# Performance work log

Measured on AMD Instinct MI355X. Metric: run time of the kernel, lower is better.

Reference implementation:

```python
import jax, jax.numpy as jnp
import numpy as np

D_MODEL = 768
BATCH = 2
N_CTX = 4096


def setup_inputs() -> dict:
    key = jax.random.key(0)
    k1, k2 = jax.random.split(key)
    x = jax.random.normal(k1, (BATCH, N_CTX, D_MODEL), dtype=jnp.float32)
    # proj: Linear(d_model, 3*d_model, bias=False); torch stores weight as [out, in]
    W_proj = jax.random.normal(k2, (3 * D_MODEL, D_MODEL), dtype=jnp.float32) * (1.0 / np.sqrt(D_MODEL))
    return {"x": x, "W_proj": W_proj}


def reference(x, W_proj):
    d = x.shape[-1]
    n_ctx = x.shape[-2]
    # qkv: [B, S, 3D] = x @ W^T (torch Linear semantics)
    qkv = jnp.einsum("bsd,ed->bse", x, W_proj)
    Q, K, V = jnp.split(qkv, 3, axis=-1)
    # additive causal mask: 0 on/below diagonal, -inf above (1 - 1/tril(ones))
    causal = jnp.tril(jnp.ones((n_ctx, n_ctx), dtype=bool))
    mask = jnp.where(causal, 0.0, -jnp.inf).astype(x.dtype)
    # NOTE: no 1/sqrt(d) scaling in the original module
    scores = jnp.einsum("bqd,bkd->bqk", Q, K) + mask
    attn = jax.nn.softmax(scores, axis=-1)
    out = x + jnp.einsum("bqk,bkd->bqd", attn, V)
    return out
```

## Files before the change

### kernel.cpp

```cpp
#include <hip/hip_runtime.h>
#include <hip/hip_bf16.h>
#include <hip/hip_fp16.h>

typedef _Float16 f16;
typedef _Float16 f16x8 __attribute__((ext_vector_type(8)));
typedef _Float16 f16x4 __attribute__((ext_vector_type(4)));
typedef _Float16 f16x2 __attribute__((ext_vector_type(2)));
typedef float f32x4 __attribute__((ext_vector_type(4)));

#define D_MODEL 768
#define S_CTX   4096
#define NBATCH  2
#define M_TOK   (NBATCH * S_CTX)
#define N3      (3 * D_MODEL)

__device__ __forceinline__ void gload_lds16(const void* g, void* l) {
  __builtin_amdgcn_global_load_lds(
      (__attribute__((address_space(1))) unsigned int*)g,
      (__attribute__((address_space(3))) unsigned int*)l, 16, 0, 0);
}

__global__ __launch_bounds__(256) void cvt_f32_f16(const float* __restrict__ s,
                                                   f16* __restrict__ d, int n4) {
  int i = blockIdx.x * 256 + threadIdx.x;
  if (i >= n4) return;
  f32x4 v = ((const f32x4*)s)[i];
  f16x4 h;
  h[0] = (f16)v[0]; h[1] = (f16)v[1]; h[2] = (f16)v[2]; h[3] = (f16)v[3];
  ((f16x4*)d)[i] = h;
}

__global__ __launch_bounds__(256, 2) void proj_gemm(
    const f16* __restrict__ A, const f16* __restrict__ B,
    f16* __restrict__ qh, f16* __restrict__ kh, f16* __restrict__ vth) {
  __shared__ f16 As[128 * 32];
  __shared__ f16 Bs[128 * 32];

  const int tid  = threadIdx.x;
  const int w    = tid >> 6, lane = tid & 63;
  const int wr   = w >> 1,   wc   = w & 1;
  const int bm0  = blockIdx.x * 128, bn0 = blockIdx.y * 128;
  const int srow = lane >> 2;
  const int scol = (lane & 3) * 8;

  f32x4 acc[4][4] = {};

  const f16* gA = A + (size_t)bm0 * 768;
  const f16* gB = B + (size_t)bn0 * 768;

  for (int kt = 0; kt < 24; ++kt) {
    __syncthreads();
    const int k0 = kt * 32 + scol;
#pragma unroll
    for (int cc = 0; cc < 2; ++cc) {
      int c = w + cc * 4;
      gload_lds16(gA + (size_t)(c * 16 + srow) * 768 + k0, (char*)As + c * 1024);
      gload_lds16(gB + (size_t)(c * 16 + srow) * 768 + k0, (char*)Bs + c * 1024);
    }
    __syncthreads();

    const int fr = lane & 15, fk = (lane >> 4) * 8;
    f16x8 af[4], bf[4];
#pragma unroll
    for (int i = 0; i < 4; ++i)
      af[i] = *(const f16x8*)(As + (wr * 64 + i * 16 + fr) * 32 + fk);
#pragma unroll
    for (int j = 0; j < 4; ++j)
      bf[j] = *(const f16x8*)(Bs + (wc * 64 + j * 16 + fr) * 32 + fk);
#pragma unroll
    for (int i = 0; i < 4; ++i)
#pragma unroll
      for (int j = 0; j < 4; ++j)
        acc[i][j] = __builtin_amdgcn_mfma_f32_16x16x32_f16(af[i], bf[j], acc[i][j], 0, 0, 0);
  }

  const int fr = lane & 15, fq = lane >> 4;
#pragma unroll
  for (int i = 0; i < 4; ++i) {
#pragma unroll
    for (int j = 0; j < 4; ++j) {
      int gn      = bn0 + wc * 64 + j * 16 + fr;
      int gm_base = bm0 + wr * 64 + i * 16 + fq * 4;
      if (gn < 1536) {
        f16* dst = (gn < 768) ? qh : kh;
        int  col = (gn < 768) ? gn : gn - 768;
#pragma unroll
        for (int r = 0; r < 4; ++r)
          dst[(size_t)(gm_base + r) * 768 + col] = (f16)acc[i][j][r];
      } else {
        int d = gn - 1536;
        int bb = gm_base >> 12, s = gm_base & 4095;
        f16x4 h;
        h[0] = (f16)acc[i][j][0]; h[1] = (f16)acc[i][j][1];
        h[2] = (f16)acc[i][j][2]; h[3] = (f16)acc[i][j][3];
        *(f16x4*)(vth + ((size_t)bb * 768 + d) * 4096 + s) = h;
      }
    }
  }
}

#define SM_K0   0
#define SM_K1   49152
#define SM_V    98304
#define SM_SS   147456
#define SM_PS   155648
#define SM_M    157696
#define SM_L    157824
#define SM_F    157952
#define SM_SZ   158080

__global__ __launch_bounds__(512, 2) void attn_part(
    const f16* __restrict__ qg, const f16* __restrict__ kg,
    const f16* __restrict__ vt, f16* __restrict__ p0,
    float* __restrict__ p1, float* __restrict__ ml) {
  extern __shared__ __align__(16) char smem[];
  char*  Kb0 = smem + SM_K0;
  char*  Kb1 = smem + SM_K1;
  char*  Vb  = smem + SM_V;
  float* Ss0 = (float*)(smem + SM_SS);
  float* Ss1 = Ss0 + 1024;
  char*  Ps  = smem + SM_PS;
  float* mS  = (float*)(smem + SM_M);
  float* lS  = (float*)(smem + SM_L);
  float* fS  = (float*)(smem + SM_F);

  const int tid  = threadIdx.x;
  const int wv   = tid >> 6, lane = tid & 63;
  const int fr   = lane & 15, fq = lane >> 4;
  const int qi   = wv >> 2, ki = (wv >> 1) & 1, dh = wv & 1;

  const int u = blockIdx.x;
  int vv = (u < 256) ? u : (u - 256);
  const int qb = ((u < 256) ? 127 : 63) - (vv >> 2);
  const int b  = (vv >> 1) & 1;
  const int c  = vv & 1;
  const int q0 = qb * 32;
  const int n  = (q0 >> 5) + 1;
  const int n0 = (n + 1) >> 1;
  const int ts = c ? n0 : 0;
  const int te = c ? n : n0;

  const char* kbase = (const char*)(kg + (size_t)b * 4096 * 768);
  const char* vbase = (const char*)(vt + (size_t)b * 768 * 4096);

  f16x8 qreg[12];
  {
    const f16* qp = qg + ((size_t)b * 4096 + q0 + qi * 16 + fr) * 768 + dh * 384 + fq * 8;
#pragma unroll
    for (int kk = 0; kk < 12; ++kk) qreg[kk] = *(const f16x8*)(qp + kk * 32);
  }

  if (tid < 32) { mS[tid] = -1e30f; lS[tid] = 0.f; }

  f32x4 acc[2][6] = {};

  if (ts < te) {
    const char* kb = kbase + (size_t)(ts * 32) * 1536;
    char* dst = (ts & 1) ? Kb1 : Kb0;
#pragma unroll
    for (int i = 0; i < 6; ++i) {
      int lin = wv * 6144 + i * 1024 + lane * 16;
      int row = lin / 1536, cb = lin - row * 1536;
      gload_lds16(kb + (size_t)row * 1536 + (cb ^ ((row & 7) << 4)),
                  dst + wv * 6144 + i * 1024);
    }
  }
  asm volatile("s_waitcnt vmcnt(0)" ::: "memory");
  __builtin_amdgcn_s_barrier();

  for (int t = ts; t < te; ++t) {
    const int kv0 = t * 32;
    const bool pf = (t + 1 < te);

    {
      const char* vb = vbase + (size_t)kv0 * 2;
#pragma unroll
      for (int i = 0; i < 6; ++i) {
        int lin = wv * 6144 + i * 1024 + lane * 16;
        int d = lin >> 6, cb = lin & 63;
        gload_lds16(vb + (size_t)d * 8192 + (cb ^ (((d >> 1) & 3) << 4)),
                    Vb + wv * 6144 + i * 1024);
      }
    }
    if (pf) {
      const char* kb = kbase + (size_t)(kv0 + 32) * 1536;
      char* dst = ((t + 1) & 1) ? Kb1 : Kb0;
#pragma unroll
      for (int i = 0; i < 6; ++i) {
        int lin = wv * 6144 + i * 1024 + lane * 16;
        int row = lin / 1536, cb = lin - row * 1536;
        gload_lds16(kb + (size_t)row * 1536 + (cb ^ ((row & 7) << 4)),
                    dst + wv * 6144 + i * 1024);
      }
    }

    {
      const char* kbuf = (t & 1) ? Kb1 : Kb0;
      f32x4 sc = {};
      const int krow = ki * 16 + fr;
      const int kswz = (krow & 7) << 4;
      __builtin_amdgcn_s_setprio(1);
#pragma unroll
      for (int kk = 0; kk < 12; ++kk) {
        int by = krow * 1536 + dh * 768 + kk * 64 + fq * 16;
        f16x8 kf = *(const f16x8*)(kbuf + (by ^ kswz));
        sc = __builtin_amdgcn_mfma_f32_16x16x32_f16(qreg[kk], kf, sc, 0, 0, 0);
      }
      __builtin_amdgcn_s_setprio(0);
      float* sdst = (dh ? Ss1 : Ss0) + (qi * 16 + fq * 4) * 32 + ki * 16 + fr;
#pragma unroll
      for (int r = 0; r < 4; ++r) sdst[r * 32] = sc[r];
    }
    asm volatile("s_waitcnt lgkmcnt(0)" ::: "memory");
    __builtin_amdgcn_s_barrier();

    {
      const int row = tid >> 4, sub = tid & 15;
      const int c0 = sub * 2;
      float a0 = Ss0[row * 32 + c0]     + Ss1[row * 32 + c0];
      float a1 = Ss0[row * 32 + c0 + 1] + Ss1[row * 32 + c0 + 1];
      const int grow = q0 + row;
      if (kv0 + c0     > grow) a0 = -1e30f;
      if (kv0 + c0 + 1 > grow) a1 = -1e30f;
      float mx = fmaxf(a0, a1);
      mx = fmaxf(mx, __shfl_xor(mx, 1));
      mx = fmaxf(mx, __shfl_xor(mx, 2));
      mx = fmaxf(mx, __shfl_xor(mx, 4));
      mx = fmaxf(mx, __shfl_xor(mx, 8));
      float mo = mS[row];
      float mn = fmaxf(mo, mx);
      float p0v = __expf(a0 - mn), p1v = __expf(a1 - mn);
      float sum = p0v + p1v;
      sum += __shfl_xor(sum, 1);
      sum += __shfl_xor(sum, 2);
      sum += __shfl_xor(sum, 4);
      sum += __shfl_xor(sum, 8);
      if (sub == 0) {
        float f = __expf(mo - mn);
        mS[row] = mn; fS[row] = f; lS[row] = lS[row] * f + sum;
      }
      f16x2 ph; ph[0] = (f16)p0v; ph[1] = (f16)p1v;
      int by = row * 64 + sub * 4;
      *(f16x2*)(Ps + (by ^ (((row >> 1) & 3) << 4))) = ph;
    }
    asm volatile("s_waitcnt lgkmcnt(0)" ::: "memory");
    __builtin_amdgcn_s_barrier();

    {
      f32x4 f0 = *(const f32x4*)(fS + fq * 4);
      f32x4 f1 = *(const f32x4*)(fS + 16 + fq * 4);
#pragma unroll
      for (int ct = 0; ct < 6; ++ct)
#pragma unroll
        for (int r = 0; r < 4; ++r) {
          acc[0][ct][r] *= f0[r];
          acc[1][ct][r] *= f1[r];
        }
      int byA0 = (fr * 64 + fq * 16) ^ (((fr >> 1) & 3) << 4);
      int rb = 16 + fr;
      int byA1 = (rb * 64 + fq * 16) ^ (((rb >> 1) & 3) << 4);
      f16x8 pa0 = *(const f16x8*)(Ps + byA0);
      f16x8 pa1 = *(const f16x8*)(Ps + byA1);
      if (pf) { asm volatile("s_waitcnt vmcnt(6)" ::: "memory"); }
      else    { asm volatile("s_waitcnt vmcnt(0)" ::: "memory"); }
      __builtin_amdgcn_s_setprio(1);
#pragma unroll
      for (int ct = 0; ct < 6; ++ct) {
        int d = wv * 96 + ct * 16 + fr;
        int by = (d * 64 + fq * 16) ^ (((d >> 1) & 3) << 4);
        f16x8 bv = *(const f16x8*)(Vb + by);
        acc[0][ct] = __builtin_amdgcn_mfma_f32_16x16x32_f16(pa0, bv, acc[0][ct], 0, 0, 0);
        acc[1][ct] = __builtin_amdgcn_mfma_f32_16x16x32_f16(pa1, bv, acc[1][ct], 0, 0, 0);
      }
      __builtin_amdgcn_s_setprio(0);
    }
    asm volatile("s_waitcnt vmcnt(0) lgkmcnt(0)" ::: "memory");
    __builtin_amdgcn_s_barrier();
  }

  const size_t obase = (size_t)b * 4096 + q0;
  if (c == 0) {
#pragma unroll
    for (int ct = 0; ct < 6; ++ct) {
      int d = wv * 96 + ct * 16 + fr;
#pragma unroll
      for (int r = 0; r < 4; ++r) {
        p0[(obase + fq * 4 + r) * 768 + d]      = (f16)acc[0][ct][r];
        p0[(obase + 16 + fq * 4 + r) * 768 + d] = (f16)acc[1][ct][r];
      }
    }
  } else {
#pragma unroll
    for (int ct = 0; ct < 6; ++ct) {
      int d = wv * 96 + ct * 16 + fr;
#pragma unroll
      for (int r = 0; r < 4; ++r) {
        p1[(obase + fq * 4 + r) * 768 + d]      = acc[0][ct][r];
        p1[(obase + 16 + fq * 4 + r) * 768 + d] = acc[1][ct][r];
      }
    }
  }
  if (tid < 32) {
    float* mlp = ml + ((size_t)(c * 2 + b) * 4096 + q0 + tid) * 2;
    mlp[0] = mS[tid];
    mlp[1] = lS[tid];
  }
}

__global__ __launch_bounds__(256) void attn_combine(
    const float* __restrict__ x, const f16* __restrict__ p0,
    const float* __restrict__ ml, float* __restrict__ out) {
  int i = blockIdx.x * 256 + threadIdx.x;
  int row = i / 192;
  int b = row >> 12, s = row & 4095;
  const float* m0p = ml + ((size_t)b * 4096 + s) * 2;
  const float* m1p = ml + ((size_t)(2 + b) * 4096 + s) * 2;
  float m0 = m0p[0], l0 = m0p[1];
  float m1 = m1p[0], l1 = m1p[1];
  float m  = fmaxf(m0, m1);
  float f0 = __expf(m0 - m), f1 = __expf(m1 - m);
  float inv = 1.f / (l0 * f0 + l1 * f1);
  f32x4 a1 = ((const f32x4*)out)[i];
  f16x4 a0 = ((const f16x4*)p0)[i];
  f32x4 xv = ((const f32x4*)x)[i];
  f32x4 o;
#pragma unroll
  for (int r = 0; r < 4; ++r)
    o[r] = xv[r] + ((float)a0[r] * f0 + a1[r] * f1) * inv;
  ((f32x4*)out)[i] = o;
}

extern "C" void kernel_launch(void* const* d_in, const int* in_sizes, int n_in,
                              void* d_out, int out_size, void* d_ws, size_t ws_size,
                              hipStream_t stream) {
  const float* x  = (const float*)d_in[0];
  const float* Wp = (const float*)d_in[1];
  float* out = (float*)d_out;

  char* ws = (char*)d_ws;
  f16* x_h  = (f16*)(ws);
  f16* w_h  = (f16*)(ws + 12582912);
  f16* q_h  = (f16*)(ws + 16121856);
  f16* k_h  = (f16*)(ws + 28704768);
  f16* vt_h = (f16*)(ws + 41287680);

  f16*   p0 = x_h;
  float* ml = (float*)w_h;

  hipFuncSetAttribute(reinterpret_cast<const void*>(attn_part),
                      hipFuncAttributeMaxDynamicSharedMemorySize, SM_SZ);

  cvt_f32_f16<<<(M_TOK * D_MODEL) / 1024, 256, 0, stream>>>(x, x_h, (M_TOK * D_MODEL) / 4);
  cvt_f32_f16<<<(N3 * D_MODEL) / 1024, 256, 0, stream>>>(Wp, w_h, (N3 * D_MODEL) / 4);
  proj_gemm<<<dim3(64, 18), 256, 0, stream>>>(x_h, w_h, q_h, k_h, vt_h);
  attn_part<<<512, 512, SM_SZ, stream>>>(q_h, k_h, vt_h, p0, out, ml);
  attn_combine<<<(M_TOK * D_MODEL) / 1024, 256, 0, stream>>>(x, p0, ml, out);
}
```

Before: 240.2 us.

## Software-pipeline attention loop: QK^T one tile ahead, V straight to registers

Restructures the flash-attention partial kernel so that QK^T for tile t+1 and the K prefetch for tile t+2 are issued while softmax for tile t runs. This cuts the per-iteration barriers from three to two and double-buffers the score buffer. V is no longer staged through LDS; it is loaded directly from global memory into double-buffered registers, shrinking the LDS footprint. It also splits the QK^T accumulation into two independent MFMA chains and skips the accumulator rescale when no row max changed, at the cost of more register pressure and more delicate vmcnt bookkeeping.

```diff
diff --git a/kernel.cpp b/kernel.cpp
--- a/kernel.cpp
+++ b/kernel.cpp
@@ -101,28 +101,22 @@
 
 #define SM_K0   0
 #define SM_K1   49152
-#define SM_V    98304
-#define SM_SS   147456
-#define SM_PS   155648
-#define SM_M    157696
-#define SM_L    157824
-#define SM_F    157952
-#define SM_SZ   158080
+#define SM_SS   98304
+#define SM_PS   114688
+#define SM_M    116736
+#define SM_L    116864
+#define SM_F    116992
+#define SM_SZ   117120
 
 __global__ __launch_bounds__(512, 2) void attn_part(
     const f16* __restrict__ qg, const f16* __restrict__ kg,
     const f16* __restrict__ vt, f16* __restrict__ p0,
     float* __restrict__ p1, float* __restrict__ ml) {
   extern __shared__ __align__(16) char smem[];
-  char*  Kb0 = smem + SM_K0;
-  char*  Kb1 = smem + SM_K1;
-  char*  Vb  = smem + SM_V;
-  float* Ss0 = (float*)(smem + SM_SS);
-  float* Ss1 = Ss0 + 1024;
-  char*  Ps  = smem + SM_PS;
-  float* mS  = (float*)(smem + SM_M);
-  float* lS  = (float*)(smem + SM_L);
-  float* fS  = (float*)(smem + SM_F);
+  char*  Ps = smem + SM_PS;
+  float* mS = (float*)(smem + SM_M);
+  float* lS = (float*)(smem + SM_L);
+  float* fS = (float*)(smem + SM_F);
 
   const int tid  = threadIdx.x;
   const int wv   = tid >> 6, lane = tid & 63;
@@ -141,7 +135,7 @@
   const int te = c ? n : n0;
 
   const char* kbase = (const char*)(kg + (size_t)b * 4096 * 768);
-  const char* vbase = (const char*)(vt + (size_t)b * 768 * 4096);
+  const f16*  vbase = vt + (size_t)b * 768 * 4096;
 
   f16x8 qreg[12];
   {
@@ -153,10 +147,11 @@
   if (tid < 32) { mS[tid] = -1e30f; lS[tid] = 0.f; }
 
   f32x4 acc[2][6] = {};
-
-  if (ts < te) {
-    const char* kb = kbase + (size_t)(ts * 32) * 1536;
-    char* dst = (ts & 1) ? Kb1 : Kb0;
+  f16x8 vA[6], vB[6];
+
+  auto stageK = [&](int t) {
+    const char* kb = kbase + (size_t)(t * 32) * 1536;
+    char* dst = smem + ((t & 1) ? SM_K1 : SM_K0);
 #pragma unroll
     for (int i = 0; i < 6; ++i) {
       int lin = wv * 6144 + i * 1024 + lane * 16;
@@ -164,118 +159,128 @@
       gload_lds16(kb + (size_t)row * 1536 + (cb ^ ((row & 7) << 4)),
                   dst + wv * 6144 + i * 1024);
     }
-  }
-  asm volatile("s_waitcnt vmcnt(0)" ::: "memory");
-  __builtin_amdgcn_s_barrier();
-
-  for (int t = ts; t < te; ++t) {
+  };
+
+  auto loadV = [&](int t, f16x8 (&vr)[6]) {
+    const f16* vp = vbase + (size_t)(wv * 96 + fr) * 4096 + t * 32 + fq * 8;
+#pragma unroll
+    for (int ct = 0; ct < 6; ++ct)
+      vr[ct] = *(const f16x8*)(vp + (size_t)ct * 16 * 4096);
+  };
+
+  auto qkt = [&](int t) {
+    const char* kb = smem + ((t & 1) ? SM_K1 : SM_K0);
+    const int krow = ki * 16 + fr;
+    const int kswz = (krow & 7) << 4;
+    f32x4 sa = {}, sb = {};
+#pragma unroll
+    for (int kk = 0; kk < 12; kk += 2) {
+      int by = krow * 1536 + dh * 768 + kk * 64 + fq * 16;
+      f16x8 k0 = *(const f16x8*)(kb + (by ^ kswz));
+      f16x8 k1 = *(const f16x8*)(kb + ((by + 64) ^ kswz));
+      sa = __builtin_amdgcn_mfma_f32_16x16x32_f16(qreg[kk],     k0, sa, 0, 0, 0);
+      sb = __builtin_amdgcn_mfma_f32_16x16x32_f16(qreg[kk + 1], k1, sb, 0, 0, 0);
+    }
+    sa = sa + sb;
+    float* sdst = (float*)(smem + SM_SS + ((t & 1) ? 8192 : 0) + dh * 4096)
+                  + (qi * 16 + fq * 4) * 32 + ki * 16 + fr;
+#pragma unroll
+    for (int r = 0; r < 4; ++r) sdst[r * 32] = sa[r];
+  };
+
+  auto softmax_f = [&](int t) {
     const int kv0 = t * 32;
-    const bool pf = (t + 1 < te);
-
-    {
-      const char* vb = vbase + (size_t)kv0 * 2;
-#pragma unroll
-      for (int i = 0; i < 6; ++i) {
-        int lin = wv * 6144 + i * 1024 + lane * 16;
-        int d = lin >> 6, cb = lin & 63;
-        gload_lds16(vb + (size_t)d * 8192 + (cb ^ (((d >> 1) & 3) << 4)),
-                    Vb + wv * 6144 + i * 1024);
-      }
-    }
-    if (pf) {
-      const char* kb = kbase + (size_t)(kv0 + 32) * 1536;
-      char* dst = ((t + 1) & 1) ? Kb1 : Kb0;
-#pragma unroll
-      for (int i = 0; i < 6; ++i) {
-        int lin = wv * 6144 + i * 1024 + lane * 16;
-        int row = lin / 1536, cb = lin - row * 1536;
-        gload_lds16(kb + (size_t)row * 1536 + (cb ^ ((row & 7) << 4)),
-                    dst + wv * 6144 + i * 1024);
-      }
-    }
-
-    {
-      const char* kbuf = (t & 1) ? Kb1 : Kb0;
-      f32x4 sc = {};
-      const int krow = ki * 16 + fr;
-      const int kswz = (krow & 7) << 4;
-      __builtin_amdgcn_s_setprio(1);
-#pragma unroll
-      for (int kk = 0; kk < 12; ++kk) {
-        int by = krow * 1536 + dh * 768 + kk * 64 + fq * 16;
-        f16x8 kf = *(const f16x8*)(kbuf + (by ^ kswz));
-        sc = __builtin_amdgcn_mfma_f32_16x16x32_f16(qreg[kk], kf, sc, 0, 0, 0);
-      }
-      __builtin_amdgcn_s_setprio(0);
-      float* sdst = (dh ? Ss1 : Ss0) + (qi * 16 + fq * 4) * 32 + ki * 16 + fr;
-#pragma unroll
-      for (int r = 0; r < 4; ++r) sdst[r * 32] = sc[r];
-    }
+    const float* S0 = (const float*)(smem + SM_SS + ((t & 1) ? 8192 : 0));
+    const float* S1 = S0 + 1024;
+    const int row = tid >> 4, sub = tid & 15;
+    const int c0 = sub * 2;
+    float a0 = S0[row * 32 + c0]     + S1[row * 32 + c0];
+    float a1 = S0[row * 32 + c0 + 1] + S1[row * 32 + c0 + 1];
+    const int grow = q0 + row;
+    if (kv0 + c0     > grow) a0 = -1e30f;
+    if (kv0 + c0 + 1 > grow) a1 = -1e30f;
+    float mx = fmaxf(a0, a1);
+    mx = fmaxf(mx, __shfl_xor(mx, 1));
+    mx = fmaxf(mx, __shfl_xor(mx, 2));
+    mx = fmaxf(mx, __shfl_xor(mx, 4));
+    mx = fmaxf(mx, __shfl_xor(mx, 8));
+    float mo = mS[row];
+    float mn = fmaxf(mo, mx);
+    float p0v = __expf(a0 - mn), p1v = __expf(a1 - mn);
+    float sum = p0v + p1v;
+    sum += __shfl_xor(sum, 1);
+    sum += __shfl_xor(sum, 2);
+    sum += __shfl_xor(sum, 4);
+    sum += __shfl_xor(sum, 8);
+    if (sub == 0) {
+      float f = __expf(mo - mn);
+      mS[row] = mn; fS[row] = f; lS[row] = lS[row] * f + sum;
+    }
+    f16x2 ph; ph[0] = (f16)p0v; ph[1] = (f16)p1v;
+    int by = row * 64 + sub * 4;
+    *(f16x2*)(Ps + (by ^ (((row >> 1) & 3) << 4))) = ph;
+  };
+
+  auto ITER = [&](int t, f16x8 (&vCon)[6], f16x8 (&vNxt)[6]) {
+    const bool haveN1 = (t + 1 < te);
+    const bool haveN2 = (t + 2 < te);
+    asm volatile("s_waitcnt vmcnt(6)" ::: "memory");
+    __builtin_amdgcn_s_barrier();
+    if (haveN2) stageK(t + 2);
+    asm volatile("" ::: "memory");
+    if (haveN1) loadV(t + 1, vNxt);
+    asm volatile("" ::: "memory");
+    if (haveN1) qkt(t + 1);
+    softmax_f(t);
     asm volatile("s_waitcnt lgkmcnt(0)" ::: "memory");
     __builtin_amdgcn_s_barrier();
-
-    {
-      const int row = tid >> 4, sub = tid & 15;
-      const int c0 = sub * 2;
-      float a0 = Ss0[row * 32 + c0]     + Ss1[row * 32 + c0];
-      float a1 = Ss0[row * 32 + c0 + 1] + Ss1[row * 32 + c0 + 1];
-      const int grow = q0 + row;
-      if (kv0 + c0     > grow) a0 = -1e30f;
-      if (kv0 + c0 + 1 > grow) a1 = -1e30f;
-      float mx = fmaxf(a0, a1);
-      mx = fmaxf(mx, __shfl_xor(mx, 1));
-      mx = fmaxf(mx, __shfl_xor(mx, 2));
-      mx = fmaxf(mx, __shfl_xor(mx, 4));
-      mx = fmaxf(mx, __shfl_xor(mx, 8));
-      float mo = mS[row];
-      float mn = fmaxf(mo, mx);
-      float p0v = __expf(a0 - mn), p1v = __expf(a1 - mn);
-      float sum = p0v + p1v;
-      sum += __shfl_xor(sum, 1);
-      sum += __shfl_xor(sum, 2);
-      sum += __shfl_xor(sum, 4);
-      sum += __shfl_xor(sum, 8);
-      if (sub == 0) {
-        float f = __expf(mo - mn);
-        mS[row] = mn; fS[row] = f; lS[row] = lS[row] * f + sum;
-      }
-      f16x2 ph; ph[0] = (f16)p0v; ph[1] = (f16)p1v;
-      int by = row * 64 + sub * 4;
-      *(f16x2*)(Ps + (by ^ (((row >> 1) & 3) << 4))) = ph;
-    }
-    asm volatile("s_waitcnt lgkmcnt(0)" ::: "memory");
-    __builtin_amdgcn_s_barrier();
-
     {
       f32x4 f0 = *(const f32x4*)(fS + fq * 4);
       f32x4 f1 = *(const f32x4*)(fS + 16 + fq * 4);
-#pragma unroll
-      for (int ct = 0; ct < 6; ++ct)
-#pragma unroll
-        for (int r = 0; r < 4; ++r) {
-          acc[0][ct][r] *= f0[r];
-          acc[1][ct][r] *= f1[r];
-        }
+      bool nd = (f0[0] < 1.f) || (f0[1] < 1.f) || (f0[2] < 1.f) || (f0[3] < 1.f) ||
+                (f1[0] < 1.f) || (f1[1] < 1.f) || (f1[2] < 1.f) || (f1[3] < 1.f);
+      if (__any(nd)) {
+#pragma unroll
+        for (int ct = 0; ct < 6; ++ct)
+#pragma unroll
+          for (int r = 0; r < 4; ++r) {
+            acc[0][ct][r] *= f0[r];
+            acc[1][ct][r] *= f1[r];
+          }
+      }
       int byA0 = (fr * 64 + fq * 16) ^ (((fr >> 1) & 3) << 4);
       int rb = 16 + fr;
       int byA1 = (rb * 64 + fq * 16) ^ (((rb >> 1) & 3) << 4);
       f16x8 pa0 = *(const f16x8*)(Ps + byA0);
       f16x8 pa1 = *(const f16x8*)(Ps + byA1);
-      if (pf) { asm volatile("s_waitcnt vmcnt(6)" ::: "memory"); }
-      else    { asm volatile("s_waitcnt vmcnt(0)" ::: "memory"); }
+      if (haveN2)      { asm volatile("s_waitcnt vmcnt(12)" ::: "memory"); }
+      else if (haveN1) { asm volatile("s_waitcnt vmcnt(6)"  ::: "memory"); }
+      else             { asm volatile("s_waitcnt vmcnt(0)"  ::: "memory"); }
       __builtin_amdgcn_s_setprio(1);
 #pragma unroll
       for (int ct = 0; ct < 6; ++ct) {
-        int d = wv * 96 + ct * 16 + fr;
-        int by = (d * 64 + fq * 16) ^ (((d >> 1) & 3) << 4);
-        f16x8 bv = *(const f16x8*)(Vb + by);
-        acc[0][ct] = __builtin_amdgcn_mfma_f32_16x16x32_f16(pa0, bv, acc[0][ct], 0, 0, 0);
-        acc[1][ct] = __builtin_amdgcn_mfma_f32_16x16x32_f16(pa1, bv, acc[1][ct], 0, 0, 0);
+        acc[0][ct] = __builtin_amdgcn_mfma_f32_16x16x32_f16(pa0, vCon[ct], acc[0][ct], 0, 0, 0);
+        acc[1][ct] = __builtin_amdgcn_mfma_f32_16x16x32_f16(pa1, vCon[ct], acc[1][ct], 0, 0, 0);
       }
       __builtin_amdgcn_s_setprio(0);
     }
-    asm volatile("s_waitcnt vmcnt(0) lgkmcnt(0)" ::: "memory");
+  };
+
+  if (ts < te) {
+    stageK(ts);
+    asm volatile("s_waitcnt vmcnt(0)" ::: "memory");
     __builtin_amdgcn_s_barrier();
+    if (ts + 1 < te) stageK(ts + 1);
+    asm volatile("" ::: "memory");
+    loadV(ts, vA);
+    asm volatile("" ::: "memory");
+    qkt(ts);
+    asm volatile("s_waitcnt lgkmcnt(0)" ::: "memory");
+  }
+
+  for (int t = ts; t < te; t += 2) {
+    ITER(t, vA, vB);
+    if (t + 1 < te) ITER(t + 1, vB, vA);
   }
 
   const size_t obase = (size_t)b * 4096 + q0;
```

New measurement: 356.3 us. +48.4%, slower.
